# Optimization experiments

Measured on AMD Instinct MI355X. Metric: run time of the kernel, lower is better.

## Reference

```python
import jax, jax.numpy as jnp
import numpy as np

N, D_IN, D_H = 8192, 512, 1024


def setup_inputs() -> dict:
    key = jax.random.key(0)
    ks = jax.random.split(key, 24)
    s = 0.02
    def W(k, o, i):
        return (jax.random.normal(k, (o, i), jnp.float32) * s)
    def b(k, o):
        return (jax.random.normal(k, (o,), jnp.float32) * s)
    inp = {}
    inp["event_times"] = jnp.sort(jax.random.uniform(ks[0], (N,), jnp.float32) * 100.0)
    inp["event_marks"] = jax.random.normal(ks[1], (N, D_IN), jnp.float32)
    inp["T"] = 100
    inp["Wp"] = W(ks[2], D_H, D_IN); inp["bp"] = b(ks[3], D_H)
    inp["Wi"] = W(ks[4], D_H, D_H); inp["bi"] = b(ks[5], D_H)
    inp["Wf"] = W(ks[6], D_H, D_H); inp["bf"] = b(ks[7], D_H)
    inp["Wo"] = W(ks[8], D_H, D_H); inp["bo"] = b(ks[9], D_H)
    inp["Wz"] = W(ks[10], D_H, D_H); inp["bz"] = b(ks[11], D_H)
    inp["Wd"] = W(ks[12], D_H, D_H); inp["bd"] = b(ks[13], D_H)
    inp["Ui"] = W(ks[14], D_H, D_H)
    inp["Uf"] = W(ks[15], D_H, D_H)
    inp["Uo"] = W(ks[16], D_H, D_H)
    inp["Uz"] = W(ks[17], D_H, D_H)
    inp["Ud"] = W(ks[18], D_H, D_H)
    return inp


def reference(event_times, event_marks, T, Wp, bp, Wi, bi, Wf, bf, Wo, bo, Wz, bz, Wd, bd, Ui, Uf, Uo, Uz, Ud):
    # Batched input-side GEMMs (x depends only on marks, not on recurrent state)
    X = event_marks @ Wp.T + bp                 # [N, H]
    gxi = X @ Wi.T + bi
    gxf = X @ Wf.T + bf
    gxo = X @ Wo.T + bo
    gxz = X @ Wz.T + bz
    gxd = X @ Wd.T + bd
    # dt[0] = 0: first step sees zero decay (prev_decay is zeros anyway)
    dts = jnp.concatenate([jnp.zeros((1,), X.dtype), jnp.diff(event_times)])

    def step(carry, inp):
        h, c, cb, pdec = carry
        xi, xf, xo, xz, xd, dt = inp
        # exponential cell decay toward c_bar since last event
        c = cb + (c - cb) * jnp.exp(-pdec * dt)
        ig = jax.nn.sigmoid(xi + h @ Ui.T)
        fg = jax.nn.sigmoid(xf + h @ Uf.T)
        og = jax.nn.sigmoid(xo + h @ Uo.T)
        z = jnp.tanh(xz + h @ Uz.T)
        c_new = fg * c + ig * z
        cb = fg * cb + ig * z
        dec = jax.nn.softplus(xd + h @ Ud.T)
        h = og * jnp.tanh(c_new)
        return (h, c_new, cb, dec), (h, c_new, dec)

    z0 = jnp.zeros((D_H,), X.dtype)
    (_, _, cb_final, _), (H, C, Dec) = jax.lax.scan(
        step, (z0, z0, z0, z0), (gxi, gxf, gxo, gxz, gxd, dts))
    return H, C, Dec, cb_final
```

## Files before the change

kernel.cpp:

```cpp
#include <hip/hip_runtime.h>
#include <hip/hip_bf16.h>
#include <stdint.h>

#define NSTEPS 8192
#define DH 1024
#define DIN 512
#define G5 5120
#define NHOUT ((size_t)NSTEPS * DH)

#define NBLK 128
#define DPB 8
#define WROWS 40
#define THREADS 320
#define WSTR 1048

typedef __attribute__((ext_vector_type(8))) __bf16 bf16x8;
typedef __attribute__((ext_vector_type(4))) float f32x4;
typedef __attribute__((ext_vector_type(4))) unsigned int u32x4;
typedef __attribute__((ext_vector_type(2))) unsigned int u32x2;

#if __has_builtin(__builtin_amdgcn_fdot2_f32_bf16)
#define HAVE_DOT2 1
typedef __attribute__((ext_vector_type(2))) short s16x2;
__device__ __forceinline__ s16x2 asp(unsigned int u) {
  union { unsigned int i; s16x2 s; } v;
  v.i = u;
  return v.s;
}
#else
#define HAVE_DOT2 0
#endif

__device__ __forceinline__ float bfbits2f(unsigned int u) {
  union { unsigned int i; float f; } v;
  v.i = u << 16;
  return v.f;
}
__device__ __forceinline__ float bfhi2f(unsigned int u) {
  union { unsigned int i; float f; } v;
  v.i = u & 0xffff0000u;
  return v.f;
}
__device__ __forceinline__ unsigned short f2bfbits(float f) {
  union { __bf16 b; unsigned short u; } v;
  v.b = (__bf16)f;
  return v.u;
}

__global__ void cvt_f32_bf16(const float* __restrict__ src,
                             unsigned short* __restrict__ dst, int n4) {
  int i = blockIdx.x * blockDim.x + threadIdx.x;
  int stride = gridDim.x * blockDim.x;
  for (; i < n4; i += stride) {
    float4 v = ((const float4*)src)[i];
    ushort4 o;
    o.x = f2bfbits(v.x);
    o.y = f2bfbits(v.y);
    o.z = f2bfbits(v.z);
    o.w = f2bfbits(v.w);
    ((ushort4*)dst)[i] = o;
  }
}

#define BM 128
#define BN 128
#define BK 32
#define PSTR 40

__global__ __launch_bounds__(256) void gemm_bt(
    const unsigned short* __restrict__ A,
    const unsigned short* __restrict__ Bt,
    const float* __restrict__ bias,
    unsigned short* __restrict__ C,
    int M, int N, int K, int permute) {
  __shared__ unsigned short As[BM * PSTR];
  __shared__ unsigned short Bs[BM * PSTR];
  const int tid = threadIdx.x;
  const int nbn = N / BN;
  const int m0 = (blockIdx.x / nbn) * BM;
  const int n0 = (blockIdx.x % nbn) * BN;
  const int w = tid >> 6;
  const int l = tid & 63;
  const int ln = l & 15;
  const int k8 = l >> 4;
  const int wr = (w >> 1) * 64;
  const int wc = (w & 1) * 64;
  const int row_a = tid >> 2;
  const int c8 = (tid & 3) * 8;

  f32x4 acc[4][4];
#pragma unroll
  for (int a = 0; a < 4; a++)
#pragma unroll
    for (int b = 0; b < 4; b++) acc[a][b] = f32x4{0.f, 0.f, 0.f, 0.f};

  for (int k0 = 0; k0 < K; k0 += BK) {
    uint4 a0 = *(const uint4*)(A + (size_t)(m0 + row_a) * K + k0 + c8);
    uint4 a1 = *(const uint4*)(A + (size_t)(m0 + row_a + 64) * K + k0 + c8);
    uint4 b0 = *(const uint4*)(Bt + (size_t)(n0 + row_a) * K + k0 + c8);
    uint4 b1 = *(const uint4*)(Bt + (size_t)(n0 + row_a + 64) * K + k0 + c8);
    __syncthreads();
    *(uint4*)(As + row_a * PSTR + c8) = a0;
    *(uint4*)(As + (row_a + 64) * PSTR + c8) = a1;
    *(uint4*)(Bs + row_a * PSTR + c8) = b0;
    *(uint4*)(Bs + (row_a + 64) * PSTR + c8) = b1;
    __syncthreads();
    bf16x8 af[4], bfr[4];
#pragma unroll
    for (int mi = 0; mi < 4; mi++)
      af[mi] = *(const bf16x8*)(As + (wr + mi * 16 + ln) * PSTR + k8 * 8);
#pragma unroll
    for (int ni = 0; ni < 4; ni++)
      bfr[ni] = *(const bf16x8*)(Bs + (wc + ni * 16 + ln) * PSTR + k8 * 8);
#pragma unroll
    for (int mi = 0; mi < 4; mi++)
#pragma unroll
      for (int ni = 0; ni < 4; ni++)
        acc[mi][ni] = __builtin_amdgcn_mfma_f32_16x16x32_bf16(
            af[mi], bfr[ni], acc[mi][ni], 0, 0, 0);
  }
#pragma unroll
  for (int ni = 0; ni < 4; ni++) {
    int n = n0 + wc + ni * 16 + ln;
    float bv = bias[n];
#pragma unroll
    for (int mi = 0; mi < 4; mi++) {
#pragma unroll
      for (int r = 0; r < 4; r++) {
        int m = m0 + wr + mi * 16 + k8 * 4 + r;
        size_t ci;
        if (permute) {
          unsigned j = (unsigned)n & 1023u;
          ci = (size_t)m * N +
               (size_t)((j >> 3) * 40u + (((unsigned)n >> 10) << 3) + (j & 7u));
        } else {
          ci = (size_t)m * N + n;
        }
        C[ci] = f2bfbits(acc[mi][ni][r] + bv);
      }
    }
  }
}

__global__ __launch_bounds__(THREADS) void scan_kernel(
    const float* __restrict__ times,
    const float* __restrict__ Ui, const float* __restrict__ Uf2,
    const float* __restrict__ Uo, const float* __restrict__ Uz,
    const float* __restrict__ Ud,
    const unsigned short* __restrict__ gxp,
    unsigned int* __restrict__ hbuf,
    float* __restrict__ out) {
  __shared__ unsigned short w_lds[WROWS * WSTR];
#if HAVE_DOT2
  __shared__ unsigned int hpk[DH / 2];
#else
  __shared__ float hf[DH];
#endif
  __shared__ float s_lds[WROWS];

  const int tid = threadIdx.x;
  const int bid = blockIdx.x;
  const int j0 = bid * DPB;

  {
    const float* Us[5] = {Ui, Uf2, Uo, Uz, Ud};
    for (int idx = tid; idx < WROWS * 256; idx += THREADS) {
      int row = idx >> 8;
      int c4 = idx & 255;
      const float* src =
          Us[row >> 3] + (size_t)(j0 + (row & 7)) * DH + c4 * 4;
      float4 v = *(const float4*)src;
      ushort4 o;
      o.x = f2bfbits(v.x);
      o.y = f2bfbits(v.y);
      o.z = f2bfbits(v.z);
      o.w = f2bfbits(v.w);
      *(ushort4*)(w_lds + row * WSTR + c4 * 4) = o;
    }
  }
#if HAVE_DOT2
  for (int k = tid; k < DH / 2; k += THREADS) hpk[k] = 0u;
#else
  for (int k = tid; k < DH; k += THREADS) hf[k] = 0.f;
#endif
  float c = 0.f, cbv = 0.f, cd_reg = 0.f;
  __syncthreads();

  const int row = tid >> 3;
  const int ln8 = tid & 7;
  const unsigned short* wrp = w_lds + row * WSTR + ln8 * 8;

  for (int t = 0; t < NSTEPS; ++t) {
    float gval = 0.f;
    float tcur = 0.f;
    if (tid < WROWS)
      gval = bfbits2f((unsigned int)gxp[(size_t)t * G5 + bid * WROWS + tid]);
    if (tid < DPB) tcur = times[t];

    if (t > 0 && tid < 64) {
      const unsigned int want = (unsigned int)t;
      const u32x4* pb = (const u32x4*)(hbuf + ((t - 1) & 1) * DH) + tid;
      u32x4 A, B, C2, D2;
      for (;;) {
        asm volatile(
            "global_load_dwordx4 %0, %4, off sc1\n\t"
            "global_load_dwordx4 %1, %4, off offset:1024 sc1\n\t"
            "global_load_dwordx4 %2, %4, off offset:2048 sc1\n\t"
            "global_load_dwordx4 %3, %4, off offset:3072 sc1\n\t"
            "s_waitcnt vmcnt(0)"
            : "=&v"(A), "=&v"(B), "=&v"(C2), "=&v"(D2)
            : "v"(pb)
            : "memory");
        bool ok = (A[0] >> 16) == want && (A[1] >> 16) == want &&
                  (A[2] >> 16) == want && (A[3] >> 16) == want &&
                  (B[0] >> 16) == want && (B[1] >> 16) == want &&
                  (B[2] >> 16) == want && (B[3] >> 16) == want &&
                  (C2[0] >> 16) == want && (C2[1] >> 16) == want &&
                  (C2[2] >> 16) == want && (C2[3] >> 16) == want &&
                  (D2[0] >> 16) == want && (D2[1] >> 16) == want &&
                  (D2[2] >> 16) == want && (D2[3] >> 16) == want;
        if (__all(ok)) break;
      }
#if HAVE_DOT2
      u32x2 pA = {(A[0] & 0xffffu) | (A[1] << 16),
                  (A[2] & 0xffffu) | (A[3] << 16)};
      u32x2 pB = {(B[0] & 0xffffu) | (B[1] << 16),
                  (B[2] & 0xffffu) | (B[3] << 16)};
      u32x2 pC = {(C2[0] & 0xffffu) | (C2[1] << 16),
                  (C2[2] & 0xffffu) | (C2[3] << 16)};
      u32x2 pD = {(D2[0] & 0xffffu) | (D2[1] << 16),
                  (D2[2] & 0xffffu) | (D2[3] << 16)};
      *(u32x2*)(hpk + 2 * tid) = pA;
      *(u32x2*)(hpk + 128 + 2 * tid) = pB;
      *(u32x2*)(hpk + 256 + 2 * tid) = pC;
      *(u32x2*)(hpk + 384 + 2 * tid) = pD;
#else
      f32x4 o0 = {bfbits2f(A[0] & 0xffffu), bfbits2f(A[1] & 0xffffu),
                  bfbits2f(A[2] & 0xffffu), bfbits2f(A[3] & 0xffffu)};
      f32x4 o1 = {bfbits2f(B[0] & 0xffffu), bfbits2f(B[1] & 0xffffu),
                  bfbits2f(B[2] & 0xffffu), bfbits2f(B[3] & 0xffffu)};
      f32x4 o2 = {bfbits2f(C2[0] & 0xffffu), bfbits2f(C2[1] & 0xffffu),
                  bfbits2f(C2[2] & 0xffffu), bfbits2f(C2[3] & 0xffffu)};
      f32x4 o3 = {bfbits2f(D2[0] & 0xffffu), bfbits2f(D2[1] & 0xffffu),
                  bfbits2f(D2[2] & 0xffffu), bfbits2f(D2[3] & 0xffffu)};
      *(f32x4*)(hf + 0 + 4 * tid) = o0;
      *(f32x4*)(hf + 256 + 4 * tid) = o1;
      *(f32x4*)(hf + 512 + 4 * tid) = o2;
      *(f32x4*)(hf + 768 + 4 * tid) = o3;
#endif
    }
    __syncthreads();

    {
#if HAVE_DOT2
      float a0 = 0.f, a1 = 0.f, a2 = 0.f, a3 = 0.f;
#pragma unroll
      for (int i = 0; i < 16; i++) {
        u32x4 wv = *(const u32x4*)(wrp + i * 64);
        u32x4 hv = *(const u32x4*)(hpk + i * 32 + ln8 * 4);
        a0 = __builtin_amdgcn_fdot2_f32_bf16(asp(wv[0]), asp(hv[0]), a0, false);
        a1 = __builtin_amdgcn_fdot2_f32_bf16(asp(wv[1]), asp(hv[1]), a1, false);
        a2 = __builtin_amdgcn_fdot2_f32_bf16(asp(wv[2]), asp(hv[2]), a2, false);
        a3 = __builtin_amdgcn_fdot2_f32_bf16(asp(wv[3]), asp(hv[3]), a3, false);
      }
      float s = (a0 + a1) + (a2 + a3);
#else
      float a0 = 0.f, a1 = 0.f;
#pragma unroll
      for (int i = 0; i < 16; i++) {
        u32x4 wv = *(const u32x4*)(wrp + i * 64);
        const float* hp = hf + i * 64 + ln8 * 8;
        f32x4 h0 = *(const f32x4*)hp;
        f32x4 h1 = *(const f32x4*)(hp + 4);
        a0 += bfbits2f(wv[0] & 0xffffu) * h0[0];
        a1 += bfhi2f(wv[0]) * h0[1];
        a0 += bfbits2f(wv[1] & 0xffffu) * h0[2];
        a1 += bfhi2f(wv[1]) * h0[3];
        a0 += bfbits2f(wv[2] & 0xffffu) * h1[0];
        a1 += bfhi2f(wv[2]) * h1[1];
        a0 += bfbits2f(wv[3] & 0xffffu) * h1[2];
        a1 += bfhi2f(wv[3]) * h1[3];
      }
      float s = a0 + a1;
#endif
      s += __shfl_xor(s, 1);
      s += __shfl_xor(s, 2);
      s += __shfl_xor(s, 4);
      if (ln8 == 0) s_lds[row] = s;
    }
    __syncthreads();

    if (tid < 64) {
      const int d = tid & 7;
      float xi = __shfl(gval, d);
      float xf2 = __shfl(gval, 8 + d);
      float xo = __shfl(gval, 16 + d);
      float xz = __shfl(gval, 24 + d);
      float xd = __shfl(gval, 32 + d);
      unsigned int word = 0;
      float h = 0.f, cn = 0.f, ig = 0.f, fg = 0.f, z = 0.f, adv = 0.f;
      if (tid < DPB) {
        float si = s_lds[tid];
        float sf = s_lds[8 + tid];
        float so = s_lds[16 + tid];
        float sz = s_lds[24 + tid];
        float sd = s_lds[32 + tid];
        ig = 1.f / (1.f + __expf(-(xi + si)));
        fg = 1.f / (1.f + __expf(-(xf2 + sf)));
        float og = 1.f / (1.f + __expf(-(xo + so)));
        z = 1.f - 2.f / (__expf(2.f * (xz + sz)) + 1.f);
        cn = fg * cd_reg + ig * z;
        float th = 1.f - 2.f / (__expf(2.f * cn) + 1.f);
        h = og * th;
        adv = xd + sd;
        word =
            (((unsigned int)(t + 1) & 0xffffu) << 16) | (unsigned int)f2bfbits(h);
      }
      u32x4 pubv = {__shfl(word, 4 * tid + 0), __shfl(word, 4 * tid + 1),
                    __shfl(word, 4 * tid + 2), __shfl(word, 4 * tid + 3)};
      if (tid < 2) {
        u32x4* dst = (u32x4*)(hbuf + (t & 1) * DH + bid * DPB) + tid;
        asm volatile("global_store_dwordx4 %0, %1, off sc1" ::"v"(dst),
                     "v"(pubv)
                     : "memory");
      }
      if (tid < DPB) {
        float dec = fmaxf(adv, 0.f) + __logf(1.f + __expf(-fabsf(adv)));
        cbv = fg * cbv + ig * z;
        c = cn;
        int j = j0 + tid;
        out[(size_t)t * DH + j] = h;
        out[NHOUT + (size_t)t * DH + j] = cn;
        out[2 * NHOUT + (size_t)t * DH + j] = dec;
        float tn = times[t + (t < NSTEPS - 1 ? 1 : 0)];
        cd_reg = cbv + (cn - cbv) * __expf(-dec * (tn - tcur));
      }
    }
  }
  if (tid < DPB) out[3 * NHOUT + j0 + tid] = cbv;
}

extern "C" void kernel_launch(void* const* d_in, const int* in_sizes, int n_in,
                              void* d_out, int out_size, void* d_ws,
                              size_t ws_size, hipStream_t stream) {
  (void)in_sizes; (void)n_in; (void)out_size; (void)ws_size;
  const float* times = (const float*)d_in[0];
  const float* marks = (const float*)d_in[1];
  const float* Wp = (const float*)d_in[3];
  const float* bp = (const float*)d_in[4];
  const float* Wi = (const float*)d_in[5];
  const float* bi = (const float*)d_in[6];
  const float* Wf = (const float*)d_in[7];
  const float* bf_ = (const float*)d_in[8];
  const float* Wo = (const float*)d_in[9];
  const float* bo = (const float*)d_in[10];
  const float* Wz = (const float*)d_in[11];
  const float* bz = (const float*)d_in[12];
  const float* Wd = (const float*)d_in[13];
  const float* bd = (const float*)d_in[14];
  const float* Ui = (const float*)d_in[15];
  const float* Uf2 = (const float*)d_in[16];
  const float* Uo = (const float*)d_in[17];
  const float* Uz = (const float*)d_in[18];
  const float* Ud = (const float*)d_in[19];

  char* ws = (char*)d_ws;
  size_t off = 0;
  auto alloc = [&](size_t bytes) -> void* {
    void* p = ws + off;
    off += (bytes + 255) & ~(size_t)255;
    return p;
  };
  unsigned short* marks_bf = (unsigned short*)alloc((size_t)NSTEPS * DIN * 2);
  unsigned short* X_bf = (unsigned short*)alloc((size_t)NSTEPS * DH * 2);
  unsigned short* Wp_bf = (unsigned short*)alloc((size_t)DH * DIN * 2);
  unsigned short* W5_bf = (unsigned short*)alloc((size_t)G5 * DH * 2);
  float* bcat = (float*)alloc((size_t)G5 * 4);
  unsigned short* gxp = (unsigned short*)alloc((size_t)NSTEPS * G5 * 2);
  unsigned int* hbuf = (unsigned int*)alloc((size_t)2 * DH * 4);

  auto cvt = [&](const float* s, unsigned short* d, int n) {
    int n4 = n / 4;
    int grid = (n4 + 255) / 256;
    if (grid > 2048) grid = 2048;
    cvt_f32_bf16<<<grid, 256, 0, stream>>>(s, d, n4);
  };
  cvt(marks, marks_bf, NSTEPS * DIN);
  cvt(Wp, Wp_bf, DH * DIN);
  cvt(Wi, W5_bf + (size_t)0 * DH * DH, DH * DH);
  cvt(Wf, W5_bf + (size_t)1 * DH * DH, DH * DH);
  cvt(Wo, W5_bf + (size_t)2 * DH * DH, DH * DH);
  cvt(Wz, W5_bf + (size_t)3 * DH * DH, DH * DH);
  cvt(Wd, W5_bf + (size_t)4 * DH * DH, DH * DH);
  hipMemcpyAsync(bcat + 0 * DH, bi, DH * sizeof(float),
                 hipMemcpyDeviceToDevice, stream);
  hipMemcpyAsync(bcat + 1 * DH, bf_, DH * sizeof(float),
                 hipMemcpyDeviceToDevice, stream);
  hipMemcpyAsync(bcat + 2 * DH, bo, DH * sizeof(float),
                 hipMemcpyDeviceToDevice, stream);
  hipMemcpyAsync(bcat + 3 * DH, bz, DH * sizeof(float),
                 hipMemcpyDeviceToDevice, stream);
  hipMemcpyAsync(bcat + 4 * DH, bd, DH * sizeof(float),
                 hipMemcpyDeviceToDevice, stream);

  gemm_bt<<<(NSTEPS / BM) * (DH / BN), 256, 0, stream>>>(
      marks_bf, Wp_bf, bp, X_bf, NSTEPS, DH, DIN, 0);
  gemm_bt<<<(NSTEPS / BM) * (G5 / BN), 256, 0, stream>>>(
      X_bf, W5_bf, bcat, gxp, NSTEPS, G5, DH, 1);

  scan_kernel<<<NBLK, THREADS, 0, stream>>>(times, Ui, Uf2, Uo, Uz, Ud, gxp,
                                            hbuf, (float*)d_out);
}
```

Before: 16.15 ms.

## Keep recurrent weights in registers and specialize waves for poll, prefetch, publish

Result: slower. 19.65 ms (+21.6%).

```diff
diff --git a/kernel.cpp b/kernel.cpp
--- a/kernel.cpp
+++ b/kernel.cpp
@@ -12,7 +12,6 @@
 #define DPB 8
 #define WROWS 40
 #define THREADS 320
-#define WSTR 1048
 
 typedef __attribute__((ext_vector_type(8))) __bf16 bf16x8;
 typedef __attribute__((ext_vector_type(4))) float f32x4;
@@ -45,6 +44,9 @@
   union { __bf16 b; unsigned short u; } v;
   v.b = (__bf16)f;
   return v.u;
+}
+__device__ __forceinline__ unsigned int pk2(float lo, float hi) {
+  return (unsigned int)f2bfbits(lo) | ((unsigned int)f2bfbits(hi) << 16);
 }
 
 __global__ void cvt_f32_bf16(const float* __restrict__ src,
@@ -150,104 +152,83 @@
     const unsigned short* __restrict__ gxp,
     unsigned int* __restrict__ hbuf,
     float* __restrict__ out) {
-  __shared__ unsigned short w_lds[WROWS * WSTR];
-#if HAVE_DOT2
   __shared__ unsigned int hpk[DH / 2];
-#else
-  __shared__ float hf[DH];
-#endif
   __shared__ float s_lds[WROWS];
+  __shared__ float gx_ring[2][WROWS];
+  __shared__ float t_lds[NSTEPS];
 
   const int tid = threadIdx.x;
+  const int wid = tid >> 6;
+  const int l = tid & 63;
   const int bid = blockIdx.x;
   const int j0 = bid * DPB;
-
+  const int row = tid >> 3;
+  const int ln8 = tid & 7;
+
+  u32x4 Wreg[16];
   {
     const float* Us[5] = {Ui, Uf2, Uo, Uz, Ud};
-    for (int idx = tid; idx < WROWS * 256; idx += THREADS) {
-      int row = idx >> 8;
-      int c4 = idx & 255;
-      const float* src =
-          Us[row >> 3] + (size_t)(j0 + (row & 7)) * DH + c4 * 4;
-      float4 v = *(const float4*)src;
-      ushort4 o;
-      o.x = f2bfbits(v.x);
-      o.y = f2bfbits(v.y);
-      o.z = f2bfbits(v.z);
-      o.w = f2bfbits(v.w);
-      *(ushort4*)(w_lds + row * WSTR + c4 * 4) = o;
-    }
-  }
-#if HAVE_DOT2
+    const float* wsrc = Us[row >> 3] + (size_t)(j0 + (row & 7)) * DH + ln8 * 8;
+#pragma unroll
+    for (int i = 0; i < 16; i++) {
+      float4 a = *(const float4*)(wsrc + i * 64);
+      float4 b = *(const float4*)(wsrc + i * 64 + 4);
+      Wreg[i] = u32x4{pk2(a.x, a.y), pk2(a.z, a.w), pk2(b.x, b.y), pk2(b.z, b.w)};
+    }
+  }
+  for (int k = tid; k < NSTEPS / 4; k += THREADS)
+    ((float4*)t_lds)[k] = ((const float4*)times)[k];
   for (int k = tid; k < DH / 2; k += THREADS) hpk[k] = 0u;
-#else
-  for (int k = tid; k < DH; k += THREADS) hf[k] = 0.f;
-#endif
-  float c = 0.f, cbv = 0.f, cd_reg = 0.f;
+  if (wid == 2 && l < WROWS)
+    gx_ring[0][l] = bfbits2f((unsigned int)gxp[(size_t)0 * G5 + bid * WROWS + l]);
+  float cbv = 0.f, cd_reg = 0.f;
   __syncthreads();
 
-  const int row = tid >> 3;
-  const int ln8 = tid & 7;
-  const unsigned short* wrp = w_lds + row * WSTR + ln8 * 8;
+  unsigned short gnext = 0;
 
   for (int t = 0; t < NSTEPS; ++t) {
-    float gval = 0.f;
-    float tcur = 0.f;
-    if (tid < WROWS)
-      gval = bfbits2f((unsigned int)gxp[(size_t)t * G5 + bid * WROWS + tid]);
-    if (tid < DPB) tcur = times[t];
-
-    if (t > 0 && tid < 64) {
+    if (wid == 2 && l < WROWS) {
+      int tn = t + 1 < NSTEPS ? t + 1 : t;
+      gnext = gxp[(size_t)tn * G5 + bid * WROWS + l];
+    }
+
+    if (wid == 0 && t > 0) {
       const unsigned int want = (unsigned int)t;
-      const u32x4* pb = (const u32x4*)(hbuf + ((t - 1) & 1) * DH) + tid;
+      const u32x4* pb = (const u32x4*)(hbuf + ((t - 1) & 1) * DH) + l;
       u32x4 A, B, C2, D2;
+      bool ok0 = false, ok1 = false, ok2 = false, ok3 = false;
       for (;;) {
-        asm volatile(
-            "global_load_dwordx4 %0, %4, off sc1\n\t"
-            "global_load_dwordx4 %1, %4, off offset:1024 sc1\n\t"
-            "global_load_dwordx4 %2, %4, off offset:2048 sc1\n\t"
-            "global_load_dwordx4 %3, %4, off offset:3072 sc1\n\t"
-            "s_waitcnt vmcnt(0)"
-            : "=&v"(A), "=&v"(B), "=&v"(C2), "=&v"(D2)
-            : "v"(pb)
-            : "memory");
-        bool ok = (A[0] >> 16) == want && (A[1] >> 16) == want &&
-                  (A[2] >> 16) == want && (A[3] >> 16) == want &&
-                  (B[0] >> 16) == want && (B[1] >> 16) == want &&
-                  (B[2] >> 16) == want && (B[3] >> 16) == want &&
-                  (C2[0] >> 16) == want && (C2[1] >> 16) == want &&
-                  (C2[2] >> 16) == want && (C2[3] >> 16) == want &&
-                  (D2[0] >> 16) == want && (D2[1] >> 16) == want &&
-                  (D2[2] >> 16) == want && (D2[3] >> 16) == want;
-        if (__all(ok)) break;
-      }
-#if HAVE_DOT2
-      u32x2 pA = {(A[0] & 0xffffu) | (A[1] << 16),
-                  (A[2] & 0xffffu) | (A[3] << 16)};
-      u32x2 pB = {(B[0] & 0xffffu) | (B[1] << 16),
-                  (B[2] & 0xffffu) | (B[3] << 16)};
-      u32x2 pC = {(C2[0] & 0xffffu) | (C2[1] << 16),
-                  (C2[2] & 0xffffu) | (C2[3] << 16)};
-      u32x2 pD = {(D2[0] & 0xffffu) | (D2[1] << 16),
-                  (D2[2] & 0xffffu) | (D2[3] << 16)};
-      *(u32x2*)(hpk + 2 * tid) = pA;
-      *(u32x2*)(hpk + 128 + 2 * tid) = pB;
-      *(u32x2*)(hpk + 256 + 2 * tid) = pC;
-      *(u32x2*)(hpk + 384 + 2 * tid) = pD;
-#else
-      f32x4 o0 = {bfbits2f(A[0] & 0xffffu), bfbits2f(A[1] & 0xffffu),
-                  bfbits2f(A[2] & 0xffffu), bfbits2f(A[3] & 0xffffu)};
-      f32x4 o1 = {bfbits2f(B[0] & 0xffffu), bfbits2f(B[1] & 0xffffu),
-                  bfbits2f(B[2] & 0xffffu), bfbits2f(B[3] & 0xffffu)};
-      f32x4 o2 = {bfbits2f(C2[0] & 0xffffu), bfbits2f(C2[1] & 0xffffu),
-                  bfbits2f(C2[2] & 0xffffu), bfbits2f(C2[3] & 0xffffu)};
-      f32x4 o3 = {bfbits2f(D2[0] & 0xffffu), bfbits2f(D2[1] & 0xffffu),
-                  bfbits2f(D2[2] & 0xffffu), bfbits2f(D2[3] & 0xffffu)};
-      *(f32x4*)(hf + 0 + 4 * tid) = o0;
-      *(f32x4*)(hf + 256 + 4 * tid) = o1;
-      *(f32x4*)(hf + 512 + 4 * tid) = o2;
-      *(f32x4*)(hf + 768 + 4 * tid) = o3;
-#endif
+        if (!ok0)
+          asm volatile("global_load_dwordx4 %0, %1, off sc1"
+                       : "=&v"(A) : "v"(pb) : "memory");
+        if (!ok1)
+          asm volatile("global_load_dwordx4 %0, %1, off offset:1024 sc1"
+                       : "=&v"(B) : "v"(pb) : "memory");
+        if (!ok2)
+          asm volatile("global_load_dwordx4 %0, %1, off offset:2048 sc1"
+                       : "=&v"(C2) : "v"(pb) : "memory");
+        if (!ok3)
+          asm volatile("global_load_dwordx4 %0, %1, off offset:3072 sc1"
+                       : "=&v"(D2) : "v"(pb) : "memory");
+        asm volatile("s_waitcnt vmcnt(0)" ::: "memory");
+        ok0 = (A[0] >> 16) == want && (A[1] >> 16) == want &&
+              (A[2] >> 16) == want && (A[3] >> 16) == want;
+        ok1 = (B[0] >> 16) == want && (B[1] >> 16) == want &&
+              (B[2] >> 16) == want && (B[3] >> 16) == want;
+        ok2 = (C2[0] >> 16) == want && (C2[1] >> 16) == want &&
+              (C2[2] >> 16) == want && (C2[3] >> 16) == want;
+        ok3 = (D2[0] >> 16) == want && (D2[1] >> 16) == want &&
+              (D2[2] >> 16) == want && (D2[3] >> 16) == want;
+        if (__all(ok0 && ok1 && ok2 && ok3)) break;
+      }
+      *(u32x2*)(hpk + 2 * l) =
+          u32x2{(A[0] & 0xffffu) | (A[1] << 16), (A[2] & 0xffffu) | (A[3] << 16)};
+      *(u32x2*)(hpk + 128 + 2 * l) =
+          u32x2{(B[0] & 0xffffu) | (B[1] << 16), (B[2] & 0xffffu) | (B[3] << 16)};
+      *(u32x2*)(hpk + 256 + 2 * l) = u32x2{(C2[0] & 0xffffu) | (C2[1] << 16),
+                                           (C2[2] & 0xffffu) | (C2[3] << 16)};
+      *(u32x2*)(hpk + 384 + 2 * l) = u32x2{(D2[0] & 0xffffu) | (D2[1] << 16),
+                                           (D2[2] & 0xffffu) | (D2[3] << 16)};
     }
     __syncthreads();
 
@@ -256,30 +237,26 @@
       float a0 = 0.f, a1 = 0.f, a2 = 0.f, a3 = 0.f;
 #pragma unroll
       for (int i = 0; i < 16; i++) {
-        u32x4 wv = *(const u32x4*)(wrp + i * 64);
         u32x4 hv = *(const u32x4*)(hpk + i * 32 + ln8 * 4);
-        a0 = __builtin_amdgcn_fdot2_f32_bf16(asp(wv[0]), asp(hv[0]), a0, false);
-        a1 = __builtin_amdgcn_fdot2_f32_bf16(asp(wv[1]), asp(hv[1]), a1, false);
-        a2 = __builtin_amdgcn_fdot2_f32_bf16(asp(wv[2]), asp(hv[2]), a2, false);
-        a3 = __builtin_amdgcn_fdot2_f32_bf16(asp(wv[3]), asp(hv[3]), a3, false);
+        a0 = __builtin_amdgcn_fdot2_f32_bf16(asp(Wreg[i][0]), asp(hv[0]), a0, false);
+        a1 = __builtin_amdgcn_fdot2_f32_bf16(asp(Wreg[i][1]), asp(hv[1]), a1, false);
+        a2 = __builtin_amdgcn_fdot2_f32_bf16(asp(Wreg[i][2]), asp(hv[2]), a2, false);
+        a3 = __builtin_amdgcn_fdot2_f32_bf16(asp(Wreg[i][3]), asp(hv[3]), a3, false);
       }
       float s = (a0 + a1) + (a2 + a3);
 #else
       float a0 = 0.f, a1 = 0.f;
 #pragma unroll
       for (int i = 0; i < 16; i++) {
-        u32x4 wv = *(const u32x4*)(wrp + i * 64);
-        const float* hp = hf + i * 64 + ln8 * 8;
-        f32x4 h0 = *(const f32x4*)hp;
-        f32x4 h1 = *(const f32x4*)(hp + 4);
-        a0 += bfbits2f(wv[0] & 0xffffu) * h0[0];
-        a1 += bfhi2f(wv[0]) * h0[1];
-        a0 += bfbits2f(wv[1] & 0xffffu) * h0[2];
-        a1 += bfhi2f(wv[1]) * h0[3];
-        a0 += bfbits2f(wv[2] & 0xffffu) * h1[0];
-        a1 += bfhi2f(wv[2]) * h1[1];
-        a0 += bfbits2f(wv[3] & 0xffffu) * h1[2];
-        a1 += bfhi2f(wv[3]) * h1[3];
+        u32x4 hv = *(const u32x4*)(hpk + i * 32 + ln8 * 4);
+        a0 += bfbits2f(Wreg[i][0] & 0xffffu) * bfbits2f(hv[0] & 0xffffu);
+        a1 += bfhi2f(Wreg[i][0]) * bfhi2f(hv[0]);
+        a0 += bfbits2f(Wreg[i][1] & 0xffffu) * bfbits2f(hv[1] & 0xffffu);
+        a1 += bfhi2f(Wreg[i][1]) * bfhi2f(hv[1]);
+        a0 += bfbits2f(Wreg[i][2] & 0xffffu) * bfbits2f(hv[2] & 0xffffu);
+        a1 += bfhi2f(Wreg[i][2]) * bfhi2f(hv[2]);
+        a0 += bfbits2f(Wreg[i][3] & 0xffffu) * bfbits2f(hv[3] & 0xffffu);
+        a1 += bfhi2f(Wreg[i][3]) * bfhi2f(hv[3]);
       }
       float s = a0 + a1;
 #endif
@@ -288,56 +265,57 @@
       s += __shfl_xor(s, 4);
       if (ln8 == 0) s_lds[row] = s;
     }
+    if (wid == 2 && l < WROWS)
+      gx_ring[(t + 1) & 1][l] = bfbits2f((unsigned int)gnext);
     __syncthreads();
 
-    if (tid < 64) {
-      const int d = tid & 7;
-      float xi = __shfl(gval, d);
-      float xf2 = __shfl(gval, 8 + d);
-      float xo = __shfl(gval, 16 + d);
-      float xz = __shfl(gval, 24 + d);
-      float xd = __shfl(gval, 32 + d);
+    if (wid >= 3) {
       unsigned int word = 0;
-      float h = 0.f, cn = 0.f, ig = 0.f, fg = 0.f, z = 0.f, adv = 0.f;
-      if (tid < DPB) {
-        float si = s_lds[tid];
-        float sf = s_lds[8 + tid];
-        float so = s_lds[16 + tid];
-        float sz = s_lds[24 + tid];
-        float sd = s_lds[32 + tid];
-        ig = 1.f / (1.f + __expf(-(xi + si)));
-        fg = 1.f / (1.f + __expf(-(xf2 + sf)));
-        float og = 1.f / (1.f + __expf(-(xo + so)));
-        z = 1.f - 2.f / (__expf(2.f * (xz + sz)) + 1.f);
+      float h = 0.f, cn = 0.f, adv = 0.f, ig = 0.f, fg = 0.f, z = 0.f,
+            og = 0.f;
+      if (l < DPB) {
+        const float* gx = gx_ring[t & 1];
+        float si = s_lds[l] + gx[l];
+        float sf = s_lds[8 + l] + gx[8 + l];
+        float so = s_lds[16 + l] + gx[16 + l];
+        float sz = s_lds[24 + l] + gx[24 + l];
+        float sd = s_lds[32 + l] + gx[32 + l];
+        ig = 1.f / (1.f + __expf(-si));
+        fg = 1.f / (1.f + __expf(-sf));
+        og = 1.f / (1.f + __expf(-so));
+        z = 1.f - 2.f / (__expf(2.f * sz) + 1.f);
         cn = fg * cd_reg + ig * z;
         float th = 1.f - 2.f / (__expf(2.f * cn) + 1.f);
         h = og * th;
-        adv = xd + sd;
-        word =
-            (((unsigned int)(t + 1) & 0xffffu) << 16) | (unsigned int)f2bfbits(h);
-      }
-      u32x4 pubv = {__shfl(word, 4 * tid + 0), __shfl(word, 4 * tid + 1),
-                    __shfl(word, 4 * tid + 2), __shfl(word, 4 * tid + 3)};
-      if (tid < 2) {
-        u32x4* dst = (u32x4*)(hbuf + (t & 1) * DH + bid * DPB) + tid;
-        asm volatile("global_store_dwordx4 %0, %1, off sc1" ::"v"(dst),
-                     "v"(pubv)
-                     : "memory");
-      }
-      if (tid < DPB) {
+        adv = sd;
+        word = (((unsigned int)(t + 1) & 0xffffu) << 16) |
+               (unsigned int)f2bfbits(h);
+      }
+      if (wid == 4) {
+        u32x4 pubv = {__shfl(word, 4 * l + 0), __shfl(word, 4 * l + 1),
+                      __shfl(word, 4 * l + 2), __shfl(word, 4 * l + 3)};
+        if (l < 2) {
+          u32x4* dst = (u32x4*)(hbuf + (t & 1) * DH + bid * DPB) + l;
+          asm volatile("global_store_dwordx4 %0, %1, off sc1" ::"v"(dst),
+                       "v"(pubv)
+                       : "memory");
+        }
+      }
+      if (l < DPB) {
         float dec = fmaxf(adv, 0.f) + __logf(1.f + __expf(-fabsf(adv)));
         cbv = fg * cbv + ig * z;
-        c = cn;
-        int j = j0 + tid;
-        out[(size_t)t * DH + j] = h;
-        out[NHOUT + (size_t)t * DH + j] = cn;
-        out[2 * NHOUT + (size_t)t * DH + j] = dec;
-        float tn = times[t + (t < NSTEPS - 1 ? 1 : 0)];
-        cd_reg = cbv + (cn - cbv) * __expf(-dec * (tn - tcur));
-      }
-    }
-  }
-  if (tid < DPB) out[3 * NHOUT + j0 + tid] = cbv;
+        float dtn = t_lds[t + (t < NSTEPS - 1 ? 1 : 0)] - t_lds[t];
+        cd_reg = cbv + (cn - cbv) * __expf(-dec * dtn);
+        if (wid == 3) {
+          int j = j0 + l;
+          out[(size_t)t * DH + j] = h;
+          out[NHOUT + (size_t)t * DH + j] = cn;
+          out[2 * NHOUT + (size_t)t * DH + j] = dec;
+        }
+      }
+    }
+  }
+  if (wid == 3 && l < DPB) out[3 * NHOUT + j0 + l] = cbv;
 }
 
 extern "C" void kernel_launch(void* const* d_in, const int* in_sizes, int n_in,
```
